# Optimization experiments

Hardware: AMD Instinct MI355X
Metric: run time of the kernel (lower is better)

## Reference

```python
import jax, jax.numpy as jnp
import numpy as np

N_FRAMES = 64
N_ATOMS = 512
SEG_LEN = 1


def get_segments(n_atoms: int, length: int) -> np.ndarray:
    """All ordered pairs of chain segments (i,i+L),(j,j+L) that share no atoms (j-i>L)."""
    starts = np.arange(n_atoms - length)
    i, j = np.meshgrid(starts, starts, indexing='ij')
    mask = (j - i) > length
    i, j = i[mask], j[mask]
    return np.stack([i, i + length, j, j + length], axis=1).astype(np.int32)


def setup_inputs() -> dict:
    key = jax.random.key(0)
    xyz = jax.random.normal(key, (N_FRAMES, N_ATOMS, 3), dtype=jnp.float32)
    segments = jnp.asarray(get_segments(N_ATOMS, SEG_LEN))  # (P, 4) int32
    return {"xyz": xyz, "segments": segments}


def _unit(v):
    return v / jnp.linalg.norm(v, axis=-1, keepdims=True)


def reference(xyz, segments):
    # xyz: (F, N, 3); segments: (P, 4) = [i, i+L, j, j+L]
    p1 = xyz[:, segments[:, 0]]  # (F, P, 3)
    p2 = xyz[:, segments[:, 1]]
    p3 = xyz[:, segments[:, 2]]
    p4 = xyz[:, segments[:, 3]]

    r12 = p2 - p1
    r13 = p3 - p1
    r14 = p4 - p1
    r23 = p3 - p2
    r24 = p4 - p2
    r34 = p4 - p3

    # unit normals of the four faces of the tetrahedron spanned by the segment pair
    n1 = _unit(jnp.cross(r13, r14))
    n2 = _unit(jnp.cross(r14, r24))
    n3 = _unit(jnp.cross(r24, r23))
    n4 = _unit(jnp.cross(r23, r13))

    def asin_dot(a, b):
        return jnp.arcsin(jnp.clip(jnp.sum(a * b, axis=-1), -1.0, 1.0))

    # Gauss linking integral (Klenin & Langowski) per segment pair
    theta = asin_dot(n1, n2) + asin_dot(n2, n3) + asin_dot(n3, n4) + asin_dot(n4, n1)
    sign = jnp.sign(jnp.sum(jnp.cross(r34, r12) * r13, axis=-1))
    wr = theta * sign / (2.0 * jnp.pi)  # (F, P)
    return wr
```

## Files before the change

### kernel.cpp

```cpp
#include <hip/hip_runtime.h>
#include <math.h>

#define NFRAMES 64
#define NATOMS  512
#define NSEG    129795
#define NROWS   509
#define BLOCK   256
#define RUN     4

typedef float v2 __attribute__((ext_vector_type(2)));
typedef float f4u __attribute__((ext_vector_type(4), aligned(4)));

__device__ __forceinline__ v2 v2s(float x) { v2 r; r.x = x; r.y = x; return r; }
__device__ __forceinline__ v2 v2mk(float a, float b) { v2 r; r.x = a; r.y = b; return r; }
__device__ __forceinline__ v2 vfma(v2 a, v2 b, v2 c) { return __builtin_elementwise_fma(a, b, c); }
__device__ __forceinline__ v2 vabs(v2 x) { v2 r; r.x = fabsf(x.x); r.y = fabsf(x.y); return r; }
__device__ __forceinline__ v2 vmin1(v2 a) { v2 r; r.x = fminf(a.x, 1.0f); r.y = fminf(a.y, 1.0f); return r; }
__device__ __forceinline__ v2 vsqrt_raw(v2 x) {
    v2 r; r.x = __builtin_amdgcn_sqrtf(x.x); r.y = __builtin_amdgcn_sqrtf(x.y); return r;
}
__device__ __forceinline__ v2 vrsq_raw(v2 x) {
    v2 r; r.x = __builtin_amdgcn_rsqf(x.x); r.y = __builtin_amdgcn_rsqf(x.y); return r;
}
__device__ __forceinline__ v2 vcopysign(v2 m, v2 s) {
    v2 r; r.x = copysignf(m.x, s.x); r.y = copysignf(m.y, s.y); return r;
}

__device__ __forceinline__ v2 vasin(v2 x) {
    v2 ax = vmin1(vabs(x));
    v2 p  = vfma(ax, v2s(-0.156582f), v2s(1.565019f));
    v2 r  = v2s(1.57079632679f) - vsqrt_raw(v2s(1.0f) - ax) * p;
    return vcopysign(r, x);
}

struct v23 { v2 x, y, z; };

__device__ __forceinline__ v23 vcross(v23 a, v23 b) {
    return v23{ vfma(a.y, b.z, -(a.z * b.y)),
                vfma(a.z, b.x, -(a.x * b.z)),
                vfma(a.x, b.y, -(a.y * b.x)) };
}
__device__ __forceinline__ v2 vdot(v23 a, v23 b) {
    return vfma(a.x, b.x, vfma(a.y, b.y, a.z * b.z));
}

__device__ __forceinline__ int b2(int a) { return 3 * a + (a >> 2); }
#define LDS_V2 1680

__global__ __launch_bounds__(BLOCK, 4) void writhe_kernel(
    const float* __restrict__ xyz,
    float*       __restrict__ out)
{
    __shared__ v2 sp[LDS_V2];

    const int f0 = blockIdx.y * 2;
    const float* fxa = xyz + (size_t)f0 * (NATOMS * 3);
    const float* fxb = fxa + NATOMS * 3;
    for (int a = threadIdx.x; a < NATOMS; a += BLOCK) {
        const float* g0 = fxa + 3 * a;
        const float* g1 = fxb + 3 * a;
        const int s = b2(a);
        sp[s + 0] = v2mk(g0[0], g1[0]);
        sp[s + 1] = v2mk(g0[1], g1[1]);
        sp[s + 2] = v2mk(g0[2], g1[2]);
    }
    if (threadIdx.x < 3) {
        const int s = b2(NATOMS + threadIdx.x);
        sp[s + 0] = v2s(0.f); sp[s + 1] = v2s(0.f); sp[s + 2] = v2s(0.f);
    }
    __syncthreads();

    const int q  = blockIdx.x * 2 + (threadIdx.x >> 7);
    const int t  = threadIdx.x & 127;

    int rowA, rowB, lenB;
    if (q < 253)       { rowA = q + 2; rowB = 508 - q; lenB = q + 1; }
    else if (q == 253) { rowA = 1;     rowB = 0;       lenB = 0;     }
    else if (q == 254) { rowA = 0;     rowB = 0;       lenB = 0;     }
    else               { rowA = 255;   rowB = 0;       lenB = 0;     }
    const int lenA = NROWS - rowA;
    const int na   = (lenA + 3) >> 2;

    const bool inA = (t < na);
    const int row  = inA ? rowA : rowB;
    const int len  = inA ? lenA : lenB;
    const int k0   = (inA ? t : (t - na)) << 2;
    if (k0 >= len) return;

    const int j0 = row + 2 + k0;

    v2 Ax[RUN + 1], Ay[RUN + 1], Az[RUN + 1];
    #pragma unroll
    for (int m = 0; m <= RUN; ++m) {
        const int s = b2(j0 + m);
        Ax[m] = sp[s]; Ay[m] = sp[s + 1]; Az[m] = sp[s + 2];
    }
    const int sP1 = b2(row), sP2 = b2(row + 1);
    const v2 P1x = sp[sP1], P1y = sp[sP1 + 1], P1z = sp[sP1 + 2];
    const v2 P2x = sp[sP2], P2y = sp[sP2 + 1], P2z = sp[sP2 + 2];

    v23 u[RUN + 1], w34[RUN];
    #pragma unroll
    for (int m = 0; m <= RUN; ++m)
        u[m] = v23{Ax[m] - P1x, Ay[m] - P1y, Az[m] - P1z};
    #pragma unroll
    for (int m = 0; m < RUN; ++m)
        w34[m] = v23{Ax[m+1] - Ax[m], Ay[m+1] - Ay[m], Az[m+1] - Az[m]};
    const v23 s12{P2x - P1x, P2y - P1y, P2z - P1z};

    v23 vvc{u[0].x - s12.x, u[0].y - s12.y, u[0].z - s12.z};

    v23 h  = vcross(u[0], vvc);
    v2 in4 = vrsq_raw(vdot(h, h));

    const int off   = NROWS * row - (row * (row - 1)) / 2;
    const int base0 = f0 * NSEG + off + k0;
    const int rem   = len - k0;

    v2 wr_[RUN];

    #pragma unroll
    for (int k = 0; k < RUN; ++k) {
        v23 vvn{u[k+1].x - s12.x, u[k+1].y - s12.y, u[k+1].z - s12.z};
        v23 c1 = vcross(u[k], u[k + 1]);
        v23 c2 = vcross(u[k + 1], vvn);
        v23 c3 = vcross(vvn, vvc);

        v2 in1 = vrsq_raw(vdot(c1, c1));
        v2 in2 = vrsq_raw(vdot(c2, c2));
        v2 in3 = vrsq_raw(vdot(c3, c3));

        v2 d12 = vdot(c1, c2) * (in1 * in2);
        v2 d23 = vdot(c2, c3) * (in2 * in3);
        v2 e34 = vdot(c3, h)  * (in3 * in4);
        v2 e41 = vdot(h, c1)  * (in4 * in1);

        v2 theta = (vasin(d12) + vasin(d23)) - (vasin(e34) + vasin(e41));

        v2 sv = vdot(vcross(w34[k], s12), u[k]);
        v2 wr = theta * vcopysign(v2s(0.15915494309189535f), sv);
        wr.x = (sv.x == 0.0f) ? 0.0f : wr.x;
        wr.y = (sv.y == 0.0f) ? 0.0f : wr.y;
        wr_[k] = wr;

        vvc = vvn; h = c2; in4 = in2;
    }

    if (rem >= RUN) {
        f4u vx; vx.x = wr_[0].x; vx.y = wr_[1].x; vx.z = wr_[2].x; vx.w = wr_[3].x;
        f4u vy; vy.x = wr_[0].y; vy.y = wr_[1].y; vy.z = wr_[2].y; vy.w = wr_[3].y;
        *reinterpret_cast<f4u*>(out + base0)        = vx;
        *reinterpret_cast<f4u*>(out + base0 + NSEG) = vy;
    } else {
        #pragma unroll
        for (int k = 0; k < RUN; ++k)
            if (k < rem) {
                out[base0 + k]        = wr_[k].x;
                out[base0 + k + NSEG] = wr_[k].y;
            }
    }
}

extern "C" void kernel_launch(void* const* d_in, const int* in_sizes, int n_in,
                              void* d_out, int out_size, void* d_ws, size_t ws_size,
                              hipStream_t stream) {
    const float* xyz = (const float*)d_in[0];
    float*       out = (float*)d_out;

    dim3 grid(128, NFRAMES / 2);
    writhe_kernel<<<grid, BLOCK, 0, stream>>>(xyz, out);
}
```

Baseline: 82.91 us.

## Halve per-thread run length, double grid, and vectorize LDS staging

Cuts the number of consecutive segment pairs each thread computes from four to two. Each block now covers one row pair instead of two, and the grid doubles so all pairs stay covered. Staging loads coordinates as float2 with one pass per thread, and the launch-bounds occupancy hint goes from 4 to 5. This gives more parallelism and lower register pressure, but repeats more of the shared per-row setup and issues narrower stores.

```diff
diff --git a/kernel.cpp b/kernel.cpp
--- a/kernel.cpp
+++ b/kernel.cpp
@@ -6,10 +6,10 @@
 #define NSEG    129795
 #define NROWS   509
 #define BLOCK   256
-#define RUN     4
+#define RUN     2
 
 typedef float v2 __attribute__((ext_vector_type(2)));
-typedef float f4u __attribute__((ext_vector_type(4), aligned(4)));
+typedef float f2u __attribute__((ext_vector_type(2), aligned(4)));
 
 __device__ __forceinline__ v2 v2s(float x) { v2 r; r.x = x; r.y = x; return r; }
 __device__ __forceinline__ v2 v2mk(float a, float b) { v2 r; r.x = a; r.y = b; return r; }
@@ -47,31 +47,35 @@
 __device__ __forceinline__ int b2(int a) { return 3 * a + (a >> 2); }
 #define LDS_V2 1680
 
-__global__ __launch_bounds__(BLOCK, 4) void writhe_kernel(
+__global__ __launch_bounds__(BLOCK, 5) void writhe_kernel(
     const float* __restrict__ xyz,
     float*       __restrict__ out)
 {
     __shared__ v2 sp[LDS_V2];
 
     const int f0 = blockIdx.y * 2;
-    const float* fxa = xyz + (size_t)f0 * (NATOMS * 3);
-    const float* fxb = fxa + NATOMS * 3;
-    for (int a = threadIdx.x; a < NATOMS; a += BLOCK) {
-        const float* g0 = fxa + 3 * a;
-        const float* g1 = fxb + 3 * a;
-        const int s = b2(a);
-        sp[s + 0] = v2mk(g0[0], g1[0]);
-        sp[s + 1] = v2mk(g0[1], g1[1]);
-        sp[s + 2] = v2mk(g0[2], g1[2]);
+    {
+        const v2* pa = (const v2*)(xyz + (size_t)f0 * (NATOMS * 3));
+        const v2* pb = pa + (NATOMS * 3) / 2;
+        const int t3 = 3 * threadIdx.x;
+        const v2 la0 = pa[t3], la1 = pa[t3 + 1], la2 = pa[t3 + 2];
+        const v2 lb0 = pb[t3], lb1 = pb[t3 + 1], lb2 = pb[t3 + 2];
+        const int s0 = 6 * threadIdx.x + (threadIdx.x >> 1);
+        sp[s0 + 0] = v2mk(la0.x, lb0.x);
+        sp[s0 + 1] = v2mk(la0.y, lb0.y);
+        sp[s0 + 2] = v2mk(la1.x, lb1.x);
+        sp[s0 + 3] = v2mk(la1.y, lb1.y);
+        sp[s0 + 4] = v2mk(la2.x, lb2.x);
+        sp[s0 + 5] = v2mk(la2.y, lb2.y);
     }
-    if (threadIdx.x < 3) {
+    if (threadIdx.x < 2) {
         const int s = b2(NATOMS + threadIdx.x);
         sp[s + 0] = v2s(0.f); sp[s + 1] = v2s(0.f); sp[s + 2] = v2s(0.f);
     }
     __syncthreads();
 
-    const int q  = blockIdx.x * 2 + (threadIdx.x >> 7);
-    const int t  = threadIdx.x & 127;
+    const int q  = blockIdx.x;
+    const int t  = threadIdx.x;
 
     int rowA, rowB, lenB;
     if (q < 253)       { rowA = q + 2; rowB = 508 - q; lenB = q + 1; }
@@ -79,12 +83,12 @@
     else if (q == 254) { rowA = 0;     rowB = 0;       lenB = 0;     }
     else               { rowA = 255;   rowB = 0;       lenB = 0;     }
     const int lenA = NROWS - rowA;
-    const int na   = (lenA + 3) >> 2;
+    const int na   = (lenA + 1) >> 1;
 
     const bool inA = (t < na);
     const int row  = inA ? rowA : rowB;
     const int len  = inA ? lenA : lenB;
-    const int k0   = (inA ? t : (t - na)) << 2;
+    const int k0   = (inA ? t : (t - na)) << 1;
     if (k0 >= len) return;
 
     const int j0 = row + 2 + k0;
@@ -147,17 +151,13 @@
     }
 
     if (rem >= RUN) {
-        f4u vx; vx.x = wr_[0].x; vx.y = wr_[1].x; vx.z = wr_[2].x; vx.w = wr_[3].x;
-        f4u vy; vy.x = wr_[0].y; vy.y = wr_[1].y; vy.z = wr_[2].y; vy.w = wr_[3].y;
-        *reinterpret_cast<f4u*>(out + base0)        = vx;
-        *reinterpret_cast<f4u*>(out + base0 + NSEG) = vy;
+        f2u vx; vx.x = wr_[0].x; vx.y = wr_[1].x;
+        f2u vy; vy.x = wr_[0].y; vy.y = wr_[1].y;
+        *reinterpret_cast<f2u*>(out + base0)        = vx;
+        *reinterpret_cast<f2u*>(out + base0 + NSEG) = vy;
     } else {
-        #pragma unroll
-        for (int k = 0; k < RUN; ++k)
-            if (k < rem) {
-                out[base0 + k]        = wr_[k].x;
-                out[base0 + k + NSEG] = wr_[k].y;
-            }
+        out[base0]        = wr_[0].x;
+        out[base0 + NSEG] = wr_[0].y;
     }
 }
 
@@ -167,6 +167,6 @@
     const float* xyz = (const float*)d_in[0];
     float*       out = (float*)d_out;
 
-    dim3 grid(128, NFRAMES / 2);
+    dim3 grid(256, NFRAMES / 2);
     writhe_kernel<<<grid, BLOCK, 0, stream>>>(xyz, out);
 }
```

Result: no change. 83.94 us (+1.2%).
